# Optimization experiments

Measured on AMD Instinct MI355X. Metric: run time of the kernel, lower is better.

## Reference

```python
import jax, jax.numpy as jnp
import numpy as np

N = 50000
E = 1600000
D_IN = 256
HID = 64
HEADS = 4


def setup_inputs() -> dict:
    key = jax.random.key(0)
    ks = jax.random.split(key, 8)
    x = jax.random.normal(ks[0], (N, D_IN), dtype=jnp.float32)
    edge_index = jax.random.randint(ks[1], (2, E), 0, N, dtype=jnp.int32)
    # GATConv params (PyG default: concat=True, negative_slope=0.2, add_self_loops=True)
    W = jax.random.normal(ks[2], (D_IN, HEADS * HID), dtype=jnp.float32) * (1.0 / np.sqrt(D_IN))
    att_src = jax.random.normal(ks[3], (HEADS, HID), dtype=jnp.float32) * 0.1
    att_dst = jax.random.normal(ks[4], (HEADS, HID), dtype=jnp.float32) * 0.1
    bias = jnp.zeros((HEADS * HID,), dtype=jnp.float32)
    # fc1: Linear(hidden*4, 3)
    fc1_W = jax.random.normal(ks[5], (HEADS * HID, 3), dtype=jnp.float32) * (1.0 / np.sqrt(HEADS * HID))
    fc1_b = jnp.zeros((3,), dtype=jnp.float32)
    return {"x": x, "edge_index": edge_index, "W": W, "att_src": att_src,
            "att_dst": att_dst, "bias": bias, "fc1_W": fc1_W, "fc1_b": fc1_b}


def _gat_conv(x, edge_index, W, att_src, att_dst, bias):
    n = x.shape[0]
    xp = (x @ W).reshape(n, HEADS, HID)  # [N,H,C]
    # add self loops (PyG default)
    loops = jnp.arange(n, dtype=edge_index.dtype)
    src = jnp.concatenate([edge_index[0], loops])  # [E+N]
    dst = jnp.concatenate([edge_index[1], loops])
    a_src = jnp.sum(xp * att_src, axis=-1)  # [N,H]
    a_dst = jnp.sum(xp * att_dst, axis=-1)
    alpha = jax.nn.leaky_relu(a_src[src] + a_dst[dst], negative_slope=0.2)  # [E+N,H]
    # segment softmax over incoming edges of each dst node
    amax = jax.ops.segment_max(alpha, dst, num_segments=n)
    ex = jnp.exp(alpha - amax[dst])
    denom = jax.ops.segment_sum(ex, dst, num_segments=n)
    alpha = ex / (denom[dst] + 1e-16)
    msg = xp[src] * alpha[:, :, None]  # [E+N,H,C]
    out = jax.ops.segment_sum(msg, dst, num_segments=n)  # [N,H,C]
    return out.reshape(n, HEADS * HID) + bias


def reference(x, edge_index, W, att_src, att_dst, bias, fc1_W, fc1_b):
    # dropout is identity at inference
    h = _gat_conv(x, edge_index, W, att_src, att_dst, bias)
    h = jax.nn.leaky_relu(h, negative_slope=0.01)  # F.leaky_relu default slope
    edge_rep = h[edge_index[0]] * h[edge_index[1]] * 0.5  # [E, H*HID]
    edge_scores = edge_rep @ fc1_W + fc1_b  # [E, 3]
    return edge_scores
```

## Files before the change

kernel.cpp:

```cpp
#include <hip/hip_runtime.h>
#include <hip/hip_fp16.h>
#include <math.h>

constexpr int N    = 50000;
constexpr int E    = 1600000;
constexpr int F    = 256;
constexpr int EL   = E + N;
constexpr int NBLK = (N + 255) / 256;

typedef _Float16 v8hf __attribute__((ext_vector_type(8)));
typedef float    v4f  __attribute__((ext_vector_type(4)));

__global__ void k_cvt_x(const float* __restrict__ x, _Float16* __restrict__ xh) {
  const size_t i = ((size_t)blockIdx.x * 256 + threadIdx.x) * 4;
  const float4 v = *(const float4*)(x + i);
  _Float16 h[4] = {(_Float16)v.x, (_Float16)v.y, (_Float16)v.z, (_Float16)v.w};
  *(uint2*)(xh + i) = *(const uint2*)h;
}

__global__ void k_cvt_w(const float* __restrict__ W, _Float16* __restrict__ wt) {
  const int id = blockIdx.x * 256 + threadIdx.x;
  const int n = id >> 8, k = id & 255;
  wt[id] = (_Float16)W[k * 256 + n];
}

__global__ __launch_bounds__(256) void k_xw_mfma(
    const _Float16* __restrict__ xh, const _Float16* __restrict__ wt,
    const float* __restrict__ att_src, const float* __restrict__ att_dst,
    __half* __restrict__ xp, float* __restrict__ a_src, float* __restrict__ a_dst) {
  const int wv   = threadIdx.x >> 6;
  const int lane = threadIdx.x & 63;
  const int q = lane >> 4, l16 = lane & 15;
  const int m0 = blockIdx.x * 16;
  const int c0 = wv * 64;

  v4f acc[4] = {{0,0,0,0},{0,0,0,0},{0,0,0,0},{0,0,0,0}};
  const _Float16* arow = xh + (size_t)(m0 + l16) * 256 + q * 8;
  const _Float16* brow = wt + (size_t)(c0 + l16) * 256 + q * 8;

  for (int kc = 0; kc < 256; kc += 32) {
    const v8hf a = *(const v8hf*)(arow + kc);
    #pragma unroll
    for (int tn = 0; tn < 4; ++tn) {
      const v8hf b = *(const v8hf*)(brow + (size_t)tn * 16 * 256 + kc);
      acc[tn] = __builtin_amdgcn_mfma_f32_16x16x32_f16(a, b, acc[tn], 0, 0, 0);
    }
  }

  #pragma unroll
  for (int tn = 0; tn < 4; ++tn) {
    const int col = c0 + tn * 16 + l16;
    #pragma unroll
    for (int r = 0; r < 4; ++r)
      xp[(size_t)(m0 + q * 4 + r) * 256 + col] = __float2half_rn(acc[tn][r]);
  }

  float aw[4], dw[4];
  #pragma unroll
  for (int tn = 0; tn < 4; ++tn) {
    aw[tn] = att_src[c0 + tn * 16 + l16];
    dw[tn] = att_dst[c0 + tn * 16 + l16];
  }
  #pragma unroll
  for (int r = 0; r < 4; ++r) {
    float ps = acc[0][r]*aw[0] + acc[1][r]*aw[1] + acc[2][r]*aw[2] + acc[3][r]*aw[3];
    float pd = acc[0][r]*dw[0] + acc[1][r]*dw[1] + acc[2][r]*dw[2] + acc[3][r]*dw[3];
    #pragma unroll
    for (int off = 1; off < 16; off <<= 1) {
      ps += __shfl_xor(ps, off, 16);
      pd += __shfl_xor(pd, off, 16);
    }
    if (l16 == 0) {
      a_src[(m0 + q * 4 + r) * 4 + wv] = ps;
      a_dst[(m0 + q * 4 + r) * 4 + wv] = pd;
    }
  }
}

__global__ void k_hist(const int* __restrict__ ei, int* __restrict__ counts) {
  const int i = blockIdx.x * blockDim.x + threadIdx.x;
  if (i < E) atomicAdd(&counts[ei[E + i]], 1);
}

__global__ __launch_bounds__(256) void k_scan1(
    const int* __restrict__ counts, int* __restrict__ offsets, int* __restrict__ partials) {
  __shared__ int s[256];
  const int t = threadIdx.x;
  const int i = blockIdx.x * 256 + t;
  const int v = (i < N) ? counts[i] + 1 : 0;
  s[t] = v;
  __syncthreads();
  for (int off = 1; off < 256; off <<= 1) {
    const int add = (t >= off) ? s[t - off] : 0;
    __syncthreads();
    s[t] += add;
    __syncthreads();
  }
  if (i < N) offsets[i] = s[t] - v;
  if (t == 255) partials[blockIdx.x] = s[255];
}

__global__ __launch_bounds__(256) void k_scan2(int* __restrict__ partials) {
  __shared__ int s[256];
  const int t = threadIdx.x;
  const int v = (t < NBLK) ? partials[t] : 0;
  s[t] = v;
  __syncthreads();
  for (int off = 1; off < 256; off <<= 1) {
    const int add = (t >= off) ? s[t - off] : 0;
    __syncthreads();
    s[t] += add;
    __syncthreads();
  }
  if (t < NBLK) partials[t] = s[t] - v;
}

__global__ void k_scan3(int* __restrict__ offsets, const int* __restrict__ partials,
                        int* __restrict__ cursor) {
  const int i = blockIdx.x * 256 + threadIdx.x;
  if (i < N) {
    const int v = offsets[i] + partials[blockIdx.x];
    offsets[i] = v;
    cursor[i]  = v;
  }
  if (i == 0) offsets[N] = EL;
}

__global__ void k_scatter(const int* __restrict__ ei, int* __restrict__ cursor,
                          int* __restrict__ srcs, int* __restrict__ eids) {
  const int i = blockIdx.x * blockDim.x + threadIdx.x;
  if (i >= EL) return;
  int s, d, id;
  if (i < E) { s = ei[i]; d = ei[E + i]; id = i; }
  else       { s = d = i - E; id = -1; }
  const int pos = atomicAdd(&cursor[d], 1);
  srcs[pos] = s;
  eids[pos] = id;
}

__global__ __launch_bounds__(128) void k_agg(
    const __half* __restrict__ xp, const float* __restrict__ a_src,
    const float* __restrict__ a_dst, const int* __restrict__ srcs,
    const int* __restrict__ offsets, const float* __restrict__ bias,
    __half* __restrict__ h) {
  const int n = blockIdx.x * 2 + (threadIdx.x >> 6);
  const int lane = threadIdx.x & 63;
  const int hd = lane >> 4, es = lane & 15;
  const int beg = offsets[n], end = offsets[n + 1];
  const float adst = a_dst[n * 4 + hd];
  const __half* xb = xp + (size_t)lane * 4;

  float a0 = 0.f, a1 = 0.f, a2 = 0.f, a3 = 0.f, den = 0.f;

  for (int c = beg; c < end; c += 16) {
    const int cnt = min(16, end - c);
    int sv = 0; float wvv = 0.f;
    if (es < cnt) {
      sv = srcs[c + es];
      float al = a_src[sv * 4 + hd] + adst;
      al = al > 0.f ? al : 0.2f * al;
      wvv = __expf(al);
    }
    int j = 0;
    for (; j + 4 <= cnt; j += 4) {
      const int   s0 = __shfl(sv, j + 0, 16), s1 = __shfl(sv, j + 1, 16);
      const int   s2 = __shfl(sv, j + 2, 16), s3 = __shfl(sv, j + 3, 16);
      const float w0 = __shfl(wvv, j + 0, 16), w1 = __shfl(wvv, j + 1, 16);
      const float w2 = __shfl(wvv, j + 2, 16), w3 = __shfl(wvv, j + 3, 16);
      const uint2 r0 = *(const uint2*)(xb + (size_t)s0 * 256);
      const uint2 r1 = *(const uint2*)(xb + (size_t)s1 * 256);
      const uint2 r2 = *(const uint2*)(xb + (size_t)s2 * 256);
      const uint2 r3 = *(const uint2*)(xb + (size_t)s3 * 256);
      den += (w0 + w1) + (w2 + w3);
      {
        const __half2* p = (const __half2*)&r0;
        const float2 lo = __half22float2(p[0]), hi = __half22float2(p[1]);
        a0 += w0 * lo.x; a1 += w0 * lo.y; a2 += w0 * hi.x; a3 += w0 * hi.y;
      }
      {
        const __half2* p = (const __half2*)&r1;
        const float2 lo = __half22float2(p[0]), hi = __half22float2(p[1]);
        a0 += w1 * lo.x; a1 += w1 * lo.y; a2 += w1 * hi.x; a3 += w1 * hi.y;
      }
      {
        const __half2* p = (const __half2*)&r2;
        const float2 lo = __half22float2(p[0]), hi = __half22float2(p[1]);
        a0 += w2 * lo.x; a1 += w2 * lo.y; a2 += w2 * hi.x; a3 += w2 * hi.y;
      }
      {
        const __half2* p = (const __half2*)&r3;
        const float2 lo = __half22float2(p[0]), hi = __half22float2(p[1]);
        a0 += w3 * lo.x; a1 += w3 * lo.y; a2 += w3 * hi.x; a3 += w3 * hi.y;
      }
    }
    for (; j < cnt; ++j) {
      const int   s = __shfl(sv, j, 16);
      const float w = __shfl(wvv, j, 16);
      const uint2 r = *(const uint2*)(xb + (size_t)s * 256);
      const __half2* p = (const __half2*)&r;
      const float2 lo = __half22float2(p[0]), hi = __half22float2(p[1]);
      den += w;
      a0 += w * lo.x; a1 += w * lo.y; a2 += w * hi.x; a3 += w * hi.y;
    }
  }

  const float inv = 1.f / (den + 1e-16f);
  const float4 bv = *(const float4*)(bias + lane * 4);
  float o0 = a0 * inv + bv.x, o1 = a1 * inv + bv.y;
  float o2 = a2 * inv + bv.z, o3 = a3 * inv + bv.w;
  o0 = o0 > 0.f ? o0 : 0.01f * o0;
  o1 = o1 > 0.f ? o1 : 0.01f * o1;
  o2 = o2 > 0.f ? o2 : 0.01f * o2;
  o3 = o3 > 0.f ? o3 : 0.01f * o3;
  const __half2 p0 = __floats2half2_rn(o0, o1), p1 = __floats2half2_rn(o2, o3);
  uint2 st;
  st.x = *(const unsigned*)&p0;
  st.y = *(const unsigned*)&p1;
  *(uint2*)(h + (size_t)n * 256 + lane * 4) = st;
}

__global__ __launch_bounds__(256) void k_score(
    const __half2* __restrict__ h2, const int* __restrict__ srcs,
    const int* __restrict__ eids, const int* __restrict__ offsets,
    const float* __restrict__ fc1W, const float* __restrict__ fc1b,
    float* __restrict__ out) {
  const int n = blockIdx.x * 4 + (threadIdx.x >> 6);
  const int lane = threadIdx.x & 63;
  const int sub  = lane >> 4;
  const int fl   = lane & 15;

  float w[48];
  {
    const float4* wp = (const float4*)(fc1W + fl * 48);
    #pragma unroll
    for (int j = 0; j < 12; ++j) ((float4*)w)[j] = wp[j];
  }
  const float b0 = fc1b[0], b1 = fc1b[1], b2 = fc1b[2];

  float hd[16];
  {
    const uint4* dp = (const uint4*)(h2 + (size_t)n * 128 + fl * 8);
    const uint4 d0 = dp[0], d1 = dp[1];
    const __half2* a = (const __half2*)&d0;
    const __half2* b = (const __half2*)&d1;
    #pragma unroll
    for (int j = 0; j < 4; ++j) {
      hd[2 * j]     = __low2float(a[j])  * 0.5f;
      hd[2 * j + 1] = __high2float(a[j]) * 0.5f;
      hd[8 + 2 * j]     = __low2float(b[j])  * 0.5f;
      hd[8 + 2 * j + 1] = __high2float(b[j]) * 0.5f;
    }
  }

  const int beg = offsets[n], end = offsets[n + 1];
  for (int i0 = beg; i0 < end; i0 += 4) {
    const int i = i0 + sub;
    const bool act = (i < end);
    int s = 0, eid = -1;
    if (act) { s = srcs[i]; eid = eids[i]; }

    float p0 = 0.f, p1 = 0.f, p2 = 0.f;
    if (act) {
      const uint4* sp = (const uint4*)(h2 + (size_t)s * 128 + fl * 8);
      const uint4 s0 = sp[0], s1 = sp[1];
      const __half2* a = (const __half2*)&s0;
      const __half2* b = (const __half2*)&s1;
      float hs[16];
      #pragma unroll
      for (int j = 0; j < 4; ++j) {
        hs[2 * j]     = __low2float(a[j]);
        hs[2 * j + 1] = __high2float(a[j]);
        hs[8 + 2 * j]     = __low2float(b[j]);
        hs[8 + 2 * j + 1] = __high2float(b[j]);
      }
      #pragma unroll
      for (int j = 0; j < 16; ++j) {
        const float r = hs[j] * hd[j];
        p0 += r * w[3 * j + 0];
        p1 += r * w[3 * j + 1];
        p2 += r * w[3 * j + 2];
      }
    }
    #pragma unroll
    for (int off = 1; off < 16; off <<= 1) {
      p0 += __shfl_xor(p0, off, 16);
      p1 += __shfl_xor(p1, off, 16);
      p2 += __shfl_xor(p2, off, 16);
    }
    if (act && eid >= 0 && fl == 0) {
      out[(size_t)eid * 3 + 0] = p0 + b0;
      out[(size_t)eid * 3 + 1] = p1 + b1;
      out[(size_t)eid * 3 + 2] = p2 + b2;
    }
  }
}

static inline size_t align256(size_t b) { return (b + 255) & ~(size_t)255; }

extern "C" void kernel_launch(void* const* d_in, const int* in_sizes, int n_in,
                              void* d_out, int out_size, void* d_ws, size_t ws_size,
                              hipStream_t stream) {
  const float* x    = (const float*)d_in[0];
  const int*   ei   = (const int*)  d_in[1];
  const float* W    = (const float*)d_in[2];
  const float* attS = (const float*)d_in[3];
  const float* attD = (const float*)d_in[4];
  const float* bias = (const float*)d_in[5];
  const float* fc1W = (const float*)d_in[6];
  const float* fc1b = (const float*)d_in[7];
  float*       out  = (float*)d_out;
  char*        ws   = (char*)d_ws;

  size_t off = 0;
  auto alloc = [&](size_t bytes) -> void* {
    void* p = ws + off;
    off += align256(bytes);
    return p;
  };
  _Float16* xh     = (_Float16*)alloc((size_t)N * F * sizeof(_Float16));
  _Float16* wt     = (_Float16*)alloc((size_t)F * F * sizeof(_Float16));
  __half*   xp     = (__half*)  alloc((size_t)N * F * sizeof(__half));
  __half*   hbuf   = (__half*)  alloc((size_t)N * F * sizeof(__half));
  float*    a_src  = (float*)   alloc((size_t)N * 4 * sizeof(float));
  float*    a_dst  = (float*)   alloc((size_t)N * 4 * sizeof(float));
  int*      counts = (int*)     alloc((size_t)N * sizeof(int));
  int*      offs   = (int*)     alloc((size_t)(N + 1) * sizeof(int));
  int*      partial= (int*)     alloc(256 * sizeof(int));
  int*      cursor = (int*)     alloc((size_t)N * sizeof(int));
  int*      srcs   = (int*)     alloc((size_t)EL * sizeof(int));
  int*      eids   = (int*)     alloc((size_t)EL * sizeof(int));

  hipMemsetAsync(counts, 0, (size_t)N * sizeof(int), stream);

  k_cvt_x<<<(N * F / 4 + 255) / 256, 256, 0, stream>>>(x, xh);
  k_cvt_w<<<F * F / 256, 256, 0, stream>>>(W, wt);
  k_xw_mfma<<<N / 16, 256, 0, stream>>>(xh, wt, attS, attD, xp, a_src, a_dst);
  k_hist<<<(E + 255) / 256, 256, 0, stream>>>(ei, counts);
  k_scan1<<<NBLK, 256, 0, stream>>>(counts, offs, partial);
  k_scan2<<<1, 256, 0, stream>>>(partial);
  k_scan3<<<NBLK, 256, 0, stream>>>(offs, partial, cursor);
  k_scatter<<<(EL + 255) / 256, 256, 0, stream>>>(ei, cursor, srcs, eids);
  k_agg<<<N / 2, 128, 0, stream>>>(xp, a_src, a_dst, srcs, offs, bias, hbuf);
  k_score<<<(N + 3) / 4, 256, 0, stream>>>((const __half2*)hbuf, srcs, eids, offs,
                                           fc1W, fc1b, out);
}
```

Before: 666.4 us.

## Compute edge scores with MFMA over 16-edge tiles and pack src/eid pairs

```diff
diff --git a/kernel.cpp b/kernel.cpp
--- a/kernel.cpp
+++ b/kernel.cpp
@@ -22,6 +22,12 @@
   const int id = blockIdx.x * 256 + threadIdx.x;
   const int n = id >> 8, k = id & 255;
   wt[id] = (_Float16)W[k * 256 + n];
+}
+
+__global__ void k_cvt_w3(const float* __restrict__ fc1W, _Float16* __restrict__ wt3h) {
+  const int id = blockIdx.x * 256 + threadIdx.x;
+  const int n = id >> 8, k = id & 255;
+  wt3h[id] = (n < 3) ? (_Float16)(0.5f * fc1W[k * 3 + n]) : (_Float16)0.f;
 }
 
 __global__ __launch_bounds__(256) void k_xw_mfma(
@@ -127,20 +133,19 @@
 }
 
 __global__ void k_scatter(const int* __restrict__ ei, int* __restrict__ cursor,
-                          int* __restrict__ srcs, int* __restrict__ eids) {
+                          int2* __restrict__ se) {
   const int i = blockIdx.x * blockDim.x + threadIdx.x;
   if (i >= EL) return;
   int s, d, id;
   if (i < E) { s = ei[i]; d = ei[E + i]; id = i; }
   else       { s = d = i - E; id = -1; }
   const int pos = atomicAdd(&cursor[d], 1);
-  srcs[pos] = s;
-  eids[pos] = id;
+  se[pos] = make_int2(s, id);
 }
 
 __global__ __launch_bounds__(128) void k_agg(
     const __half* __restrict__ xp, const float* __restrict__ a_src,
-    const float* __restrict__ a_dst, const int* __restrict__ srcs,
+    const float* __restrict__ a_dst, const int2* __restrict__ se,
     const int* __restrict__ offsets, const float* __restrict__ bias,
     __half* __restrict__ h) {
   const int n = blockIdx.x * 2 + (threadIdx.x >> 6);
@@ -156,7 +161,7 @@
     const int cnt = min(16, end - c);
     int sv = 0; float wvv = 0.f;
     if (es < cnt) {
-      sv = srcs[c + es];
+      sv = se[c + es].x;
       float al = a_src[sv * 4 + hd] + adst;
       al = al > 0.f ? al : 0.2f * al;
       wvv = __expf(al);
@@ -219,78 +224,57 @@
   *(uint2*)(h + (size_t)n * 256 + lane * 4) = st;
 }
 
-__global__ __launch_bounds__(256) void k_score(
-    const __half2* __restrict__ h2, const int* __restrict__ srcs,
-    const int* __restrict__ eids, const int* __restrict__ offsets,
-    const float* __restrict__ fc1W, const float* __restrict__ fc1b,
-    float* __restrict__ out) {
+__global__ __launch_bounds__(256) void k_score_mfma(
+    const _Float16* __restrict__ h, const int2* __restrict__ se,
+    const int* __restrict__ offsets, const _Float16* __restrict__ wt3h,
+    const float* __restrict__ fc1b, float* __restrict__ out) {
   const int n = blockIdx.x * 4 + (threadIdx.x >> 6);
   const int lane = threadIdx.x & 63;
-  const int sub  = lane >> 4;
-  const int fl   = lane & 15;
-
-  float w[48];
+  const int q = lane >> 4, l16 = lane & 15;
+
+  v8hf bfrag[8];
   {
-    const float4* wp = (const float4*)(fc1W + fl * 48);
-    #pragma unroll
-    for (int j = 0; j < 12; ++j) ((float4*)w)[j] = wp[j];
-  }
-  const float b0 = fc1b[0], b1 = fc1b[1], b2 = fc1b[2];
-
-  float hd[16];
+    const _Float16* brow = wt3h + l16 * 256 + q * 8;
+    #pragma unroll
+    for (int kci = 0; kci < 8; ++kci)
+      bfrag[kci] = *(const v8hf*)(brow + kci * 32);
+  }
+  v8hf hdv[8];
   {
-    const uint4* dp = (const uint4*)(h2 + (size_t)n * 128 + fl * 8);
-    const uint4 d0 = dp[0], d1 = dp[1];
-    const __half2* a = (const __half2*)&d0;
-    const __half2* b = (const __half2*)&d1;
-    #pragma unroll
-    for (int j = 0; j < 4; ++j) {
-      hd[2 * j]     = __low2float(a[j])  * 0.5f;
-      hd[2 * j + 1] = __high2float(a[j]) * 0.5f;
-      hd[8 + 2 * j]     = __low2float(b[j])  * 0.5f;
-      hd[8 + 2 * j + 1] = __high2float(b[j]) * 0.5f;
-    }
-  }
+    const _Float16* drow = h + (size_t)n * 256 + q * 8;
+    #pragma unroll
+    for (int kci = 0; kci < 8; ++kci)
+      hdv[kci] = *(const v8hf*)(drow + kci * 32);
+  }
+  const float bn = (l16 < 3) ? fc1b[l16] : 0.f;
 
   const int beg = offsets[n], end = offsets[n + 1];
-  for (int i0 = beg; i0 < end; i0 += 4) {
-    const int i = i0 + sub;
-    const bool act = (i < end);
-    int s = 0, eid = -1;
-    if (act) { s = srcs[i]; eid = eids[i]; }
-
-    float p0 = 0.f, p1 = 0.f, p2 = 0.f;
-    if (act) {
-      const uint4* sp = (const uint4*)(h2 + (size_t)s * 128 + fl * 8);
-      const uint4 s0 = sp[0], s1 = sp[1];
-      const __half2* a = (const __half2*)&s0;
-      const __half2* b = (const __half2*)&s1;
-      float hs[16];
+  for (int c = beg; c < end; c += 16) {
+    const int idx = c + l16;
+    int s = -1, eid = -1;
+    if (idx < end) { const int2 p = se[idx]; s = p.x; eid = p.y; }
+
+    v8hf av[8] = {};
+    if (s >= 0) {
+      const _Float16* srow = h + (size_t)s * 256 + q * 8;
       #pragma unroll
-      for (int j = 0; j < 4; ++j) {
-        hs[2 * j]     = __low2float(a[j]);
-        hs[2 * j + 1] = __high2float(a[j]);
-        hs[8 + 2 * j]     = __low2float(b[j]);
-        hs[8 + 2 * j + 1] = __high2float(b[j]);
-      }
-      #pragma unroll
-      for (int j = 0; j < 16; ++j) {
-        const float r = hs[j] * hd[j];
-        p0 += r * w[3 * j + 0];
-        p1 += r * w[3 * j + 1];
-        p2 += r * w[3 * j + 2];
-      }
-    }
-    #pragma unroll
-    for (int off = 1; off < 16; off <<= 1) {
-      p0 += __shfl_xor(p0, off, 16);
-      p1 += __shfl_xor(p1, off, 16);
-      p2 += __shfl_xor(p2, off, 16);
-    }
-    if (act && eid >= 0 && fl == 0) {
-      out[(size_t)eid * 3 + 0] = p0 + b0;
-      out[(size_t)eid * 3 + 1] = p1 + b1;
-      out[(size_t)eid * 3 + 2] = p2 + b2;
+      for (int kci = 0; kci < 8; ++kci)
+        av[kci] = *(const v8hf*)(srow + kci * 32);
+    }
+
+    v4f acc = {0.f, 0.f, 0.f, 0.f};
+    #pragma unroll
+    for (int kci = 0; kci < 8; ++kci) {
+      const v8hf ar = av[kci] * hdv[kci];
+      acc = __builtin_amdgcn_mfma_f32_16x16x32_f16(ar, bfrag[kci], acc, 0, 0, 0);
+    }
+
+    #pragma unroll
+    for (int r = 0; r < 4; ++r) {
+      const int m = q * 4 + r;
+      const int em = __shfl(eid, m, 16);
+      if (l16 < 3 && c + m < end && em >= 0)
+        out[(size_t)em * 3 + l16] = acc[r] + bn;
     }
   }
 }
@@ -319,6 +303,7 @@
   };
   _Float16* xh     = (_Float16*)alloc((size_t)N * F * sizeof(_Float16));
   _Float16* wt     = (_Float16*)alloc((size_t)F * F * sizeof(_Float16));
+  _Float16* wt3h   = (_Float16*)alloc((size_t)16 * F * sizeof(_Float16));
   __half*   xp     = (__half*)  alloc((size_t)N * F * sizeof(__half));
   __half*   hbuf   = (__half*)  alloc((size_t)N * F * sizeof(__half));
   float*    a_src  = (float*)   alloc((size_t)N * 4 * sizeof(float));
@@ -327,20 +312,20 @@
   int*      offs   = (int*)     alloc((size_t)(N + 1) * sizeof(int));
   int*      partial= (int*)     alloc(256 * sizeof(int));
   int*      cursor = (int*)     alloc((size_t)N * sizeof(int));
-  int*      srcs   = (int*)     alloc((size_t)EL * sizeof(int));
-  int*      eids   = (int*)     alloc((size_t)EL * sizeof(int));
+  int2*     se     = (int2*)    alloc((size_t)EL * sizeof(int2));
 
   hipMemsetAsync(counts, 0, (size_t)N * sizeof(int), stream);
 
   k_cvt_x<<<(N * F / 4 + 255) / 256, 256, 0, stream>>>(x, xh);
   k_cvt_w<<<F * F / 256, 256, 0, stream>>>(W, wt);
+  k_cvt_w3<<<16, 256, 0, stream>>>(fc1W, wt3h);
   k_xw_mfma<<<N / 16, 256, 0, stream>>>(xh, wt, attS, attD, xp, a_src, a_dst);
   k_hist<<<(E + 255) / 256, 256, 0, stream>>>(ei, counts);
   k_scan1<<<NBLK, 256, 0, stream>>>(counts, offs, partial);
   k_scan2<<<1, 256, 0, stream>>>(partial);
   k_scan3<<<NBLK, 256, 0, stream>>>(offs, partial, cursor);
-  k_scatter<<<(EL + 255) / 256, 256, 0, stream>>>(ei, cursor, srcs, eids);
-  k_agg<<<N / 2, 128, 0, stream>>>(xp, a_src, a_dst, srcs, offs, bias, hbuf);
-  k_score<<<(N + 3) / 4, 256, 0, stream>>>((const __half2*)hbuf, srcs, eids, offs,
-                                           fc1W, fc1b, out);
-}
+  k_scatter<<<(EL + 255) / 256, 256, 0, stream>>>(ei, cursor, se);
+  k_agg<<<N / 2, 128, 0, stream>>>(xp, a_src, a_dst, se, offs, bias, hbuf);
+  k_score_mfma<<<(N + 3) / 4, 256, 0, stream>>>((const _Float16*)hbuf, se, offs,
+                                                wt3h, fc1b, out);
+}
```

Result: no change. 665.0 us (-0.2%).
